# Kernel optimization log

Measured on AMD Instinct MI355X. Metric: run time of the kernel, lower is better.

## Reference

```python
import jax, jax.numpy as jnp
import numpy as np

B, H, L, N = 4, 256, 8192, 32  # batch, channels, seq_len, d_state//2 complex modes


def setup_inputs() -> dict:
    key = jax.random.key(0)
    ks = jax.random.split(key, 8)
    x = jax.random.normal(ks[0], (B, H, L), jnp.float32)
    # ChannelwiseLayerNorm params
    ln1_g = jnp.ones((H,), jnp.float32); ln1_b = jnp.zeros((H,), jnp.float32)
    ln2_g = jnp.ones((H,), jnp.float32); ln2_b = jnp.zeros((H,), jnp.float32)
    # S4D params (standard diagonal S4D init)
    log_dt = jax.random.uniform(ks[1], (H,), jnp.float32, np.log(1e-3), np.log(1e-1))
    log_A_real = jnp.log(0.5 * jnp.ones((H, N), jnp.float32))
    A_imag = jnp.tile(np.pi * jnp.arange(N, dtype=jnp.float32)[None, :], (H, 1))
    C_re = jax.random.normal(ks[2], (H, N), jnp.float32) * (0.5 ** 0.5)
    C_im = jax.random.normal(ks[3], (H, N), jnp.float32) * (0.5 ** 0.5)
    D = jax.random.normal(ks[4], (H,), jnp.float32)
    # 1x1 convs as dense matrices
    glu_w = jax.random.normal(ks[5], (2 * H, H), jnp.float32) * (1.0 / H) ** 0.5
    glu_b = jnp.zeros((2 * H,), jnp.float32)
    ffn_in_w = jax.random.normal(ks[6], (4 * H, H), jnp.float32) * (1.0 / H) ** 0.5
    ffn_in_b = jnp.zeros((4 * H,), jnp.float32)
    ffn_out_w = jax.random.normal(ks[7], (H, 4 * H), jnp.float32) * (1.0 / (4 * H)) ** 0.5
    ffn_out_b = jnp.zeros((H,), jnp.float32)
    return dict(x=x, ln1_g=ln1_g, ln1_b=ln1_b, ln2_g=ln2_g, ln2_b=ln2_b,
                log_dt=log_dt, log_A_real=log_A_real, A_imag=A_imag,
                C_re=C_re, C_im=C_im, D=D,
                glu_w=glu_w, glu_b=glu_b,
                ffn_in_w=ffn_in_w, ffn_in_b=ffn_in_b,
                ffn_out_w=ffn_out_w, ffn_out_b=ffn_out_b)


def _channel_ln(x, g, b, eps=1e-5):
    # normalize over channel dim (axis=1) of (B, C, L)
    mu = jnp.mean(x, axis=1, keepdims=True)
    var = jnp.var(x, axis=1, keepdims=True)
    return (x - mu) / jnp.sqrt(var + eps) * g[None, :, None] + b[None, :, None]


def _s4d(u, log_dt, log_A_real, A_imag, C_re, C_im, D):
    # u: (B, H, L); diagonal SSM via Vandermonde kernel + FFT conv
    Ls = u.shape[-1]
    dt = jnp.exp(log_dt)                       # (H,)
    A = -jnp.exp(log_A_real) + 1j * A_imag     # (H, N)
    dtA = A * dt[:, None]                      # (H, N)
    Cc = (C_re + 1j * C_im) * (jnp.exp(dtA) - 1.0) / A
    vand = jnp.exp(dtA[:, :, None] * jnp.arange(Ls))      # (H, N, L)
    K = 2.0 * jnp.einsum('hn,hnl->hl', Cc, vand).real     # (H, L)
    n = 2 * Ls
    y = jnp.fft.irfft(jnp.fft.rfft(u, n=n) * jnp.fft.rfft(K, n=n), n=n)[..., :Ls]
    return y + u * D[None, :, None]


def reference(x, ln1_g, ln1_b, ln2_g, ln2_b, log_dt, log_A_real, A_imag,
              C_re, C_im, D, glu_w, glu_b, ffn_in_w, ffn_in_b, ffn_out_w, ffn_out_b):
    # branch 1: norm -> S4D -> GELU -> 1x1 conv -> GLU -> residual
    y = _channel_ln(x, ln1_g, ln1_b)
    y = _s4d(y, log_dt, log_A_real, A_imag, C_re, C_im, D)
    y = jax.nn.gelu(y, approximate=False)
    y = jnp.einsum('oc,bcl->bol', glu_w, y) + glu_b[None, :, None]
    a, g = jnp.split(y, 2, axis=1)
    y = a * jax.nn.sigmoid(g)
    mid = x + y
    # branch 2: norm -> FFN (1x1 conv, GELU, 1x1 conv) -> residual
    y = _channel_ln(mid, ln2_g, ln2_b)
    y = jnp.einsum('oc,bcl->bol', ffn_in_w, y) + ffn_in_b[None, :, None]
    y = jax.nn.gelu(y, approximate=False)
    y = jnp.einsum('oc,bcl->bol', ffn_out_w, y) + ffn_out_b[None, :, None]
    return mid + y
```

## Files before the change

kernel.cpp:

```cpp
#include <hip/hip_runtime.h>
#include <hip/hip_bf16.h>

#define BB 4
#define HH 256
#define LL 8192
#define NN 32
#define CH 64
#define TT 128

typedef __attribute__((ext_vector_type(4))) float f32x4;
typedef __attribute__((ext_vector_type(8))) short s16x8;
typedef __attribute__((ext_vector_type(4))) short s16x4;
typedef unsigned int u32;

static __device__ __forceinline__ ushort f2bf(float f){
    union { float f; unsigned int i; } v; v.f = f;
    unsigned int x = v.i;
    return (ushort)((x + 0x7fffu + ((x >> 16) & 1u)) >> 16);
}

static __device__ __forceinline__ float fast_gelu(float x){
    float x3 = x*x*x;
    float z  = fmaf(0.03567740814f, x3, 0.7978845608f*x);
    float e  = __builtin_amdgcn_exp2f(z * 2.885390082f);
    float t  = 1.f - 2.f*__builtin_amdgcn_rcpf(e + 1.f);
    return 0.5f*x*(1.f + t);
}
static __device__ __forceinline__ float fast_sigmoid(float x){
    float e = __builtin_amdgcn_exp2f(-x * 1.442695041f);
    return __builtin_amdgcn_rcpf(1.f + e);
}

__global__ void k_prep_weights(const float* __restrict__ gw, const float* __restrict__ fiw,
                               const float* __restrict__ fow,
                               ushort* __restrict__ dglu, ushort* __restrict__ dfi,
                               ushort* __restrict__ dfo){
    int i = blockIdx.x * 256 + threadIdx.x;
    if (i < 512*256)  dglu[i] = f2bf(gw[i]);
    if (i < 1024*256) dfi[i]  = f2bf(fiw[i]);
    if (i < 1024*256) dfo[i]  = f2bf(fow[i]);
}

__global__ void k_scan_params(const float* __restrict__ log_dt, const float* __restrict__ log_A_real,
                              const float* __restrict__ A_imag, float4* __restrict__ out){
    int i = blockIdx.x * 256 + threadIdx.x;
    int h = i >> 5;
    float dt  = expf(log_dt[h]);
    float Are = -expf(log_A_real[i]);
    float Aim = A_imag[i];
    float xr = Are * dt, xi = Aim * dt;
    float er = expf(xr), sn, cs;
    sincosf(xi, &sn, &cs);
    float erT = expf(xr * (float)TT), snT, csT;
    sincosf(xi * (float)TT, &snT, &csT);
    out[i] = make_float4(er*cs, er*sn, erT*csT, erT*snT);
}

__global__ void __launch_bounds__(256) k_build(const float* __restrict__ log_dt,
      const float* __restrict__ log_A_real, const float* __restrict__ A_imag,
      const float* __restrict__ C_re, const float* __restrict__ C_im, const float* __restrict__ Dp,
      ushort* __restrict__ Tkb, ushort* __restrict__ M2b, ushort* __restrict__ V2b){
    int h = blockIdx.x, tid = threadIdx.x;
    __shared__ float prm[4][32];
    __shared__ float2 pw[129][32];
    __shared__ float kk[129];
    if (tid < 32){
        int n = tid, i = h*NN + n;
        float dt  = expf(log_dt[h]);
        float Are = -expf(log_A_real[i]);
        float Aim = A_imag[i];
        float xr = Are*dt, xi = Aim*dt;
        float er = expf(xr), sn, cs; sincosf(xi, &sn, &cs);
        float wre = er*cs, wim = er*sn;
        float nre = wre - 1.f, nim = wim;
        float inv = 1.f / (Are*Are + Aim*Aim);
        float qre = (nre*Are + nim*Aim) * inv;
        float qim = (nim*Are - nre*Aim) * inv;
        float cre = C_re[i], cim = C_im[i];
        prm[0][n] = xr; prm[1][n] = xi;
        prm[2][n] = 2.f*(cre*qre - cim*qim);
        prm[3][n] = 2.f*(cre*qim + cim*qre);
    }
    __syncthreads();
    if (tid < 129){
        float d = (float)tid, acc = 0.f;
        for (int n = 0; n < 32; ++n){
            float er = expf(prm[0][n]*d), sn, cs; sincosf(prm[1][n]*d, &sn, &cs);
            float pre = er*cs, pim = er*sn;
            pw[tid][n] = make_float2(pre, pim);
            acc += prm[2][n]*pre - prm[3][n]*pim;
        }
        kk[tid] = acc;
    }
    __syncthreads();
    float k0d = kk[0] + Dp[h];
    for (int idx = tid; idx < 128*128; idx += 256){
        int t = idx >> 7, ta = idx & 127, d = t - ta;
        float v = (d < 0) ? 0.f : ((d == 0) ? k0d : kk[d]);
        Tkb[(size_t)h*16384 + idx] = f2bf(v);
    }
    for (int idx = tid; idx < 128*64; idx += 256){
        int t = idx >> 6, j = idx & 63, n = j & 31;
        float2 p = pw[t+1][n];
        float v = (j < 32) ?  (prm[2][n]*p.x - prm[3][n]*p.y)
                           : -(prm[2][n]*p.y + prm[3][n]*p.x);
        M2b[(size_t)h*8192 + idx] = f2bf(v);
    }
    for (int idx = tid; idx < 64*128; idx += 256){
        int row = idx >> 7, ta = idx & 127, n = row & 31;
        float2 p = pw[127 - ta][n];
        V2b[(size_t)h*8192 + idx] = f2bf(row < 32 ? p.x : p.y);
    }
}

template<int MODE>
__global__ void __launch_bounds__(256) k_ln(const float* __restrict__ in, void* __restrict__ outp,
                     const float* __restrict__ gamma, const float* __restrict__ beta){
    int p = threadIdx.x & 63, cg = threadIdx.x >> 6;
    int b  = blockIdx.x / (LL/64);
    int l  = (blockIdx.x % (LL/64)) * 64 + p;
    const float* base = in + (size_t)b*HH*LL + l;
    int c0 = cg * 64;
    float s = 0.f, s2 = 0.f;
    #pragma unroll 8
    for (int j = 0; j < 64; ++j){
        float v = base[(size_t)(c0+j)*LL];
        s += v; s2 += v*v;
    }
    __shared__ float red[2][4][64];
    red[0][cg][p] = s; red[1][cg][p] = s2;
    __syncthreads();
    float ts = red[0][0][p]+red[0][1][p]+red[0][2][p]+red[0][3][p];
    float tq = red[1][0][p]+red[1][1][p]+red[1][2][p]+red[1][3][p];
    float mu   = ts * (1.f/HH);
    float var  = tq * (1.f/HH) - mu*mu;
    float rstd = rsqrtf(var + 1e-5f);
    if (MODE == 1){
        ushort* ob = (ushort*)outp + ((size_t)(b*LL + l))*HH + c0;
        #pragma unroll
        for (int j8 = 0; j8 < 8; ++j8){
            s16x8 v;
            #pragma unroll
            for (int e = 0; e < 8; ++e){
                int c = c0 + j8*8 + e;
                v[e] = (short)f2bf((base[(size_t)c*LL] - mu)*rstd*gamma[c] + beta[c]);
            }
            *(s16x8*)(ob + j8*8) = v;
        }
    } else {
        ushort* ob = (ushort*)outp + (size_t)b*HH*LL + l;
        #pragma unroll 8
        for (int j = 0; j < 64; ++j){
            int c = c0 + j;
            ob[(size_t)c*LL] = f2bf((base[(size_t)c*LL] - mu)*rstd*gamma[c] + beta[c]);
        }
    }
}

__global__ void __launch_bounds__(256) k_gemmA(const ushort* __restrict__ V2b,
                        const ushort* __restrict__ ub, float2* __restrict__ est){
    int bh = blockIdx.x, h = bh & (HH-1);
    int tid = threadIdx.x, wave = tid >> 6, lane = tid & 63;
    int m16 = lane & 15, kg = lane >> 4;
    const ushort* Vh = V2b + (size_t)h*8192;
    const ushort* ux = ub + (size_t)bh*LL;
    f32x4 acc[4] = {};
    #pragma unroll
    for (int k0 = 0; k0 < 128; k0 += 32){
        s16x8 fa = *(const s16x8*)&Vh[(wave*16 + m16)*128 + k0 + kg*8];
        #pragma unroll
        for (int nf = 0; nf < 4; ++nf){
            s16x8 fb = *(const s16x8*)&ux[(size_t)(nf*16 + m16)*128 + k0 + kg*8];
            acc[nf] = __builtin_amdgcn_mfma_f32_16x16x32_bf16(fa, fb, acc[nf], 0, 0, 0);
        }
    }
    #pragma unroll
    for (int nf = 0; nf < 4; ++nf){
        int c = nf*16 + m16;
        #pragma unroll
        for (int r = 0; r < 4; ++r){
            int srow = wave*16 + kg*4 + r;
            float* dst = (float*)&est[((size_t)bh*CH + c)*NN + (srow & 31)];
            dst[srow >> 5] = acc[nf][r];
        }
    }
}

__global__ void k_scan_B(const float4* __restrict__ par, const float2* __restrict__ est,
                         ushort* __restrict__ carr){
    int i = blockIdx.x * 256 + threadIdx.x;
    int n = i & 31, bh = i >> 5, h = bh & (HH-1);
    float4 p0 = par[h*NN + n];
    float wre = p0.z, wim = p0.w;
    float cre = 0.f, cim = 0.f;
    const float2* e = est + (size_t)bh*CH*NN + n;
    ushort* cb = carr + (size_t)bh*CH*64;
    for (int c = 0; c < CH; ++c){
        cb[c*64 + n]      = f2bf(cre);
        cb[c*64 + 32 + n] = f2bf(cim);
        float2 v = e[(size_t)c*NN];
        float nre = fmaf(wre, cre, fmaf(-wim, cim, v.x));
        float nim = fmaf(wre, cim, fmaf(wim, cre, v.y));
        cre = nre; cim = nim;
    }
}

__global__ void __launch_bounds__(256) k_gemmC(const ushort* __restrict__ Tkb,
                        const ushort* __restrict__ M2b, const ushort* __restrict__ ub,
                        const ushort* __restrict__ carr, ushort* __restrict__ gy){
    int bh = blockIdx.x, h = bh & (HH-1);
    int tid = threadIdx.x, wave = tid >> 6, lane = tid & 63;
    int m16 = lane & 15, kg = lane >> 4;
    const ushort* Th = Tkb + (size_t)h*16384;
    const ushort* Mh = M2b + (size_t)h*8192;
    const ushort* ux = ub + (size_t)bh*LL;
    const ushort* cb = carr + (size_t)bh*CH*64;
    f32x4 acc[2][4] = {};
    #pragma unroll
    for (int k0 = 0; k0 < 128; k0 += 32){
        s16x8 fa0 = *(const s16x8*)&Th[(size_t)(wave*32 + m16)*128 + k0 + kg*8];
        s16x8 fa1 = *(const s16x8*)&Th[(size_t)(wave*32 + 16 + m16)*128 + k0 + kg*8];
        #pragma unroll
        for (int nf = 0; nf < 4; ++nf){
            s16x8 fb = *(const s16x8*)&ux[(size_t)(nf*16 + m16)*128 + k0 + kg*8];
            acc[0][nf] = __builtin_amdgcn_mfma_f32_16x16x32_bf16(fa0, fb, acc[0][nf], 0, 0, 0);
            acc[1][nf] = __builtin_amdgcn_mfma_f32_16x16x32_bf16(fa1, fb, acc[1][nf], 0, 0, 0);
        }
    }
    #pragma unroll
    for (int k0 = 0; k0 < 64; k0 += 32){
        s16x8 fa0 = *(const s16x8*)&Mh[(wave*32 + m16)*64 + k0 + kg*8];
        s16x8 fa1 = *(const s16x8*)&Mh[(wave*32 + 16 + m16)*64 + k0 + kg*8];
        #pragma unroll
        for (int nf = 0; nf < 4; ++nf){
            s16x8 fb = *(const s16x8*)&cb[(nf*16 + m16)*64 + k0 + kg*8];
            acc[0][nf] = __builtin_amdgcn_mfma_f32_16x16x32_bf16(fa0, fb, acc[0][nf], 0, 0, 0);
            acc[1][nf] = __builtin_amdgcn_mfma_f32_16x16x32_bf16(fa1, fb, acc[1][nf], 0, 0, 0);
        }
    }
    #pragma unroll
    for (int mf = 0; mf < 2; ++mf){
        #pragma unroll
        for (int nf = 0; nf < 4; ++nf){
            int c = nf*16 + m16;
            int t0 = wave*32 + mf*16 + kg*4;
            s16x4 pk;
            #pragma unroll
            for (int r = 0; r < 4; ++r){
                pk[r] = (short)f2bf(fast_gelu(acc[mf][nf][r]));
            }
            *(s16x4*)&gy[(size_t)bh*LL + c*TT + t0] = pk;
        }
    }
}

__global__ void k_transpose(const ushort* __restrict__ in, ushort* __restrict__ out){
    __shared__ ushort tile[64][66];
    int tid = threadIdx.x;
    int lt = blockIdx.x, ht = blockIdx.y, b = blockIdx.z;
    const ushort* ib = in + ((size_t)b*HH + ht*64)*LL + lt*64;
    #pragma unroll
    for (int k = 0; k < 16; ++k){
        int j = tid + k*256;
        tile[j >> 6][j & 63] = ib[(size_t)(j >> 6)*LL + (j & 63)];
    }
    __syncthreads();
    ushort* obp = out + ((size_t)b*LL + lt*64)*HH + ht*64;
    #pragma unroll
    for (int k = 0; k < 16; ++k){
        int j = tid + k*256;
        obp[(size_t)(j >> 6)*HH + (j & 63)] = tile[j & 63][j >> 6];
    }
}

__global__ void __launch_bounds__(256) k_glu(const ushort* __restrict__ Wg, const ushort* __restrict__ Xt,
                     const float* __restrict__ x, const float* __restrict__ gb,
                     float* __restrict__ mid){
    __shared__ __align__(16) ushort sh[32768];
    int tid = threadIdx.x;
    int w = tid >> 6, lane = tid & 63;
    int m16 = lane & 15, kg = lane >> 4;
    int wr = w >> 1, wc = w & 1;
    int p0  = blockIdx.x * 128;
    int oa0 = blockIdx.y * 64;
    const ushort* Brow = Xt + (size_t)p0*256;
    int srow = lane >> 3;
    int scol = ((lane & 7) ^ (srow & 7)) * 8;
    f32x4 aa[2][4] = {}; f32x4 ag[2][4] = {};

    #define GSTAGE(buf, kt) { \
        int k0s = (kt)*64; \
        _Pragma("unroll") \
        for (int i = 0; i < 4; ++i){ \
            int rr = (w*4 + i)*8; \
            int grow = (rr < 64) ? (oa0 + rr + srow) : (256 + oa0 + (rr - 64) + srow); \
            __builtin_amdgcn_global_load_lds( \
                (const __attribute__((address_space(1))) u32*)(Wg + (size_t)grow*256 + k0s + scol), \
                (__attribute__((address_space(3))) u32*)&sh[(buf)*8192 + rr*64], 16, 0, 0); \
            __builtin_amdgcn_global_load_lds( \
                (const __attribute__((address_space(1))) u32*)(Brow + (size_t)(rr + srow)*256 + k0s + scol), \
                (__attribute__((address_space(3))) u32*)&sh[16384 + (buf)*8192 + rr*64], 16, 0, 0); \
        } }

    int buf = 0;
    GSTAGE(0, 0);
    __syncthreads();
    for (int kt = 0; kt < 4; ++kt){
        if (kt + 1 < 4) GSTAGE(buf^1, kt+1);
        #pragma unroll
        for (int k032 = 0; k032 < 64; k032 += 32){
            int c = (k032 >> 3) + kg;
            s16x8 fa[2], fg[2], fb[4];
            #pragma unroll
            for (int i = 0; i < 2; ++i){
                int ra = wr*32 + i*16 + m16;
                int rg = 64 + wr*32 + i*16 + m16;
                fa[i] = *(const s16x8*)&sh[buf*8192 + ra*64 + ((c ^ (ra & 7)) << 3)];
                fg[i] = *(const s16x8*)&sh[buf*8192 + rg*64 + ((c ^ (rg & 7)) << 3)];
            }
            #pragma unroll
            for (int i = 0; i < 4; ++i){
                int rb = wc*64 + i*16 + m16;
                fb[i] = *(const s16x8*)&sh[16384 + buf*8192 + rb*64 + ((c ^ (rb & 7)) << 3)];
            }
            #pragma unroll
            for (int mf = 0; mf < 2; ++mf){
                #pragma unroll
                for (int nf = 0; nf < 4; ++nf){
                    aa[mf][nf] = __builtin_amdgcn_mfma_f32_16x16x32_bf16(fa[mf], fb[nf], aa[mf][nf], 0, 0, 0);
                    ag[mf][nf] = __builtin_amdgcn_mfma_f32_16x16x32_bf16(fg[mf], fb[nf], ag[mf][nf], 0, 0, 0);
                }
            }
        }
        __syncthreads();
        buf ^= 1;
    }
    #undef GSTAGE

    #pragma unroll
    for (int mf = 0; mf < 2; ++mf){
        #pragma unroll
        for (int nf = 0; nf < 4; ++nf){
            int pc = p0 + wc*64 + nf*16 + m16;
            int b = pc >> 13, l = pc & (LL-1);
            #pragma unroll
            for (int r = 0; r < 4; ++r){
                int o = oa0 + wr*32 + mf*16 + kg*4 + r;
                float va  = aa[mf][nf][r] + gb[o];
                float vg  = ag[mf][nf][r] + gb[o + 256];
                float sig = fast_sigmoid(vg);
                size_t idx = ((size_t)(b*HH + o) << 13) + l;
                mid[idx] = x[idx] + va*sig;
            }
        }
    }
}

template<int KDIM, int EPI>
__global__ void __launch_bounds__(256) k_gemm_lds(const ushort* __restrict__ A,
                      const ushort* __restrict__ Bm, const float* __restrict__ bias,
                      const float* __restrict__ mid, void* __restrict__ Cout, int pbase){
    __shared__ __align__(16) ushort sh[32768];
    int tid = threadIdx.x;
    int w = tid >> 6, lane = tid & 63;
    int m16 = lane & 15, kg = lane >> 4;
    int wr = w >> 1, wc = w & 1;
    int q0  = blockIdx.x * 128;
    int oc0 = blockIdx.y * 128;
    const ushort* Arow = A  + (size_t)oc0*KDIM;
    const ushort* Brow = Bm + (size_t)q0*KDIM;
    int srow = lane >> 3;
    int scol = ((lane & 7) ^ (srow & 7)) * 8;
    f32x4 acc[4][4] = {};
    const int nK = KDIM/64;

    #define STAGE(buf, kt) { \
        int k0s = (kt)*64; \
        _Pragma("unroll") \
        for (int i = 0; i < 4; ++i){ \
            int rr = (w*4 + i)*8; \
            __builtin_amdgcn_global_load_lds( \
                (const __attribute__((address_space(1))) u32*)(Arow + (size_t)(rr + srow)*KDIM + k0s + scol), \
                (__attribute__((address_space(3))) u32*)&sh[(buf)*8192 + rr*64], 16, 0, 0); \
            __builtin_amdgcn_global_load_lds( \
                (const __attribute__((address_space(1))) u32*)(Brow + (size_t)(rr + srow)*KDIM + k0s + scol), \
                (__attribute__((address_space(3))) u32*)&sh[16384 + (buf)*8192 + rr*64], 16, 0, 0); \
        } }

    int buf = 0;
    STAGE(0, 0);
    __syncthreads();
    for (int kt = 0; kt < nK; ++kt){
        if (kt + 1 < nK) STAGE(buf^1, kt+1);
        #pragma unroll
        for (int k032 = 0; k032 < 64; k032 += 32){
            int c = (k032 >> 3) + kg;
            s16x8 af[4], bf[4];
            #pragma unroll
            for (int i = 0; i < 4; ++i){
                int ra = wr*64 + i*16 + m16;
                int rb = wc*64 + i*16 + m16;
                af[i] = *(const s16x8*)&sh[buf*8192 + ra*64 + ((c ^ (ra & 7)) << 3)];
                bf[i] = *(const s16x8*)&sh[16384 + buf*8192 + rb*64 + ((c ^ (rb & 7)) << 3)];
            }
            #pragma unroll
            for (int mf = 0; mf < 4; ++mf){
                #pragma unroll
                for (int nf = 0; nf < 4; ++nf)
                    acc[mf][nf] = __builtin_amdgcn_mfma_f32_16x16x32_bf16(af[mf], bf[nf], acc[mf][nf], 0, 0, 0);
            }
        }
        __syncthreads();
        buf ^= 1;
    }
    #undef STAGE

    if (EPI == 0){
        ushort (*lt)[136] = (ushort(*)[136])sh;
        #pragma unroll
        for (int mf = 0; mf < 4; ++mf){
            #pragma unroll
            for (int nf = 0; nf < 4; ++nf){
                int lr = wc*64 + nf*16 + m16;
                int lc = wr*64 + mf*16 + kg*4;
                s16x4 pk;
                #pragma unroll
                for (int r = 0; r < 4; ++r){
                    float v = acc[mf][nf][r] + bias[oc0 + lc + r];
                    pk[r] = (short)f2bf(fast_gelu(v));
                }
                *(s16x4*)&lt[lr][lc] = pk;
            }
        }
        __syncthreads();
        ushort* f1 = (ushort*)Cout;
        #pragma unroll
        for (int i = 0; i < 8; ++i){
            int chunk = i*256 + tid;
            int row = chunk >> 4, c16 = chunk & 15;
            s16x8 v = *(const s16x8*)&lt[row][c16*8];
            *(s16x8*)&f1[((size_t)(q0 + row) << 10) + oc0 + c16*8] = v;
        }
    } else {
        float* out = (float*)Cout;
        #pragma unroll
        for (int mf = 0; mf < 4; ++mf){
            #pragma unroll
            for (int nf = 0; nf < 4; ++nf){
                int pc = pbase + q0 + wc*64 + nf*16 + m16;
                int b = pc >> 13, l = pc & (LL-1);
                #pragma unroll
                for (int r = 0; r < 4; ++r){
                    int oc = oc0 + wr*64 + mf*16 + kg*4 + r;
                    size_t idx = ((size_t)(b*HH + oc) << 13) + l;
                    out[idx] = mid[idx] + acc[mf][nf][r] + bias[oc];
                }
            }
        }
    }
}

extern "C" void kernel_launch(void* const* d_in, const int* in_sizes, int n_in,
                              void* d_out, int out_size, void* d_ws, size_t ws_size,
                              hipStream_t stream) {
    const float* x          = (const float*)d_in[0];
    const float* ln1_g      = (const float*)d_in[1];
    const float* ln1_b      = (const float*)d_in[2];
    const float* ln2_g      = (const float*)d_in[3];
    const float* ln2_b      = (const float*)d_in[4];
    const float* log_dt     = (const float*)d_in[5];
    const float* log_A_real = (const float*)d_in[6];
    const float* A_imag     = (const float*)d_in[7];
    const float* C_re       = (const float*)d_in[8];
    const float* C_im       = (const float*)d_in[9];
    const float* Dv         = (const float*)d_in[10];
    const float* glu_w      = (const float*)d_in[11];
    const float* glu_b      = (const float*)d_in[12];
    const float* ffn_in_w   = (const float*)d_in[13];
    const float* ffn_in_b   = (const float*)d_in[14];
    const float* ffn_out_w  = (const float*)d_in[15];
    const float* ffn_out_b  = (const float*)d_in[16];
    float* out = (float*)d_out;

    char* ws = (char*)d_ws;
    const size_t MB = 1u << 20;
    float4* par  = (float4*)(ws);
    ushort* wglu = (ushort*)(ws + 256*1024);
    ushort* wfi  = (ushort*)(ws + 512*1024);
    ushort* wfo  = (ushort*)(ws + 1024*1024);
    ushort* Tkb  = (ushort*)(ws + 2*MB);
    ushort* M2b  = (ushort*)(ws + 10*MB);
    ushort* V2b  = (ushort*)(ws + 14*MB);
    ushort* ub   = (ushort*)(ws + 18*MB);
    float2* est  = (float2*)(ws + 34*MB);
    ushort* carr = (ushort*)(ws + 50*MB);
    ushort* gy   = (ushort*)(ws + 34*MB);
    ushort* gyt  = (ushort*)(ws + 50*MB);
    float*  mid  = (float*)(ws + 2*MB);
    ushort* x2t  = (ushort*)(ws + 36*MB);
    ushort* f1   = (ushort*)(ws + 52*MB);

    int G = (ws_size >= 117*MB) ? 4 : ((ws_size >= 85*MB) ? 2 : 1);

    k_prep_weights<<<1024, 256, 0, stream>>>(glu_w, ffn_in_w, ffn_out_w, wglu, wfi, wfo);
    k_scan_params<<<32, 256, 0, stream>>>(log_dt, log_A_real, A_imag, par);
    k_build<<<HH, 256, 0, stream>>>(log_dt, log_A_real, A_imag, C_re, C_im, Dv, Tkb, M2b, V2b);
    k_ln<2><<<BB*LL/64, 256, 0, stream>>>(x, ub, ln1_g, ln1_b);
    k_gemmA<<<BB*HH, 256, 0, stream>>>(V2b, ub, est);
    k_scan_B<<<BB*HH*NN/256, 256, 0, stream>>>(par, est, carr);
    k_gemmC<<<BB*HH, 256, 0, stream>>>(Tkb, M2b, ub, carr, gy);
    k_transpose<<<dim3(LL/64, HH/64, BB), 256, 0, stream>>>(gy, gyt);
    k_glu<<<dim3(BB*LL/128, 4), 256, 0, stream>>>(wglu, gyt, x, glu_b, mid);
    k_ln<1><<<BB*LL/64, 256, 0, stream>>>(mid, x2t, ln2_g, ln2_b);
    for (int b0 = 0; b0 < BB; b0 += G){
        int pbase = b0 * LL;
        k_gemm_lds<256,0><<<dim3(G*LL/128, 8), 256, 0, stream>>>(
            wfi, x2t + (size_t)pbase*256, ffn_in_b, nullptr, f1, 0);
        k_gemm_lds<1024,1><<<dim3(G*LL/128, 2), 256, 0, stream>>>(
            wfo, f1, ffn_out_b, mid, out, pbase);
    }
    (void)in_sizes; (void)n_in; (void)out_size; (void)ws_size;
}
```

Before: 304.6 us.

## Fuse FFN up and down projections into one kernel with LDS-resident hidden tile

Replaces the two tiled LDS GEMM launches (FFN-in with GELU, then FFN-out with residual) with one kernel. Each 512-thread block handles 64 positions: it computes the 1024-wide GELU hidden activations into a 128KB swizzled LDS buffer, then runs the down projection straight from LDS. This removes the global round trip of the bf16 hidden tensor and the batch-group launch loop. In exchange, operand A and B fragments are read directly from global memory without LDS staging or double buffering, and the large LDS footprint limits each CU to one block.

```diff
diff --git a/kernel.cpp b/kernel.cpp
--- a/kernel.cpp
+++ b/kernel.cpp
@@ -356,104 +356,83 @@
     }
 }
 
-template<int KDIM, int EPI>
-__global__ void __launch_bounds__(256) k_gemm_lds(const ushort* __restrict__ A,
-                      const ushort* __restrict__ Bm, const float* __restrict__ bias,
-                      const float* __restrict__ mid, void* __restrict__ Cout, int pbase){
-    __shared__ __align__(16) ushort sh[32768];
+__global__ void __launch_bounds__(512) k_ffn_fused(const ushort* __restrict__ W1,
+                      const ushort* __restrict__ W2, const ushort* __restrict__ Xt,
+                      const float* __restrict__ b1, const float* __restrict__ b2,
+                      const float* __restrict__ mid, float* __restrict__ out){
+    __shared__ __align__(16) ushort f1s[64*1024];
     int tid = threadIdx.x;
     int w = tid >> 6, lane = tid & 63;
     int m16 = lane & 15, kg = lane >> 4;
-    int wr = w >> 1, wc = w & 1;
-    int q0  = blockIdx.x * 128;
-    int oc0 = blockIdx.y * 128;
-    const ushort* Arow = A  + (size_t)oc0*KDIM;
-    const ushort* Brow = Bm + (size_t)q0*KDIM;
-    int srow = lane >> 3;
-    int scol = ((lane & 7) ^ (srow & 7)) * 8;
-    f32x4 acc[4][4] = {};
-    const int nK = KDIM/64;
-
-    #define STAGE(buf, kt) { \
-        int k0s = (kt)*64; \
-        _Pragma("unroll") \
-        for (int i = 0; i < 4; ++i){ \
-            int rr = (w*4 + i)*8; \
-            __builtin_amdgcn_global_load_lds( \
-                (const __attribute__((address_space(1))) u32*)(Arow + (size_t)(rr + srow)*KDIM + k0s + scol), \
-                (__attribute__((address_space(3))) u32*)&sh[(buf)*8192 + rr*64], 16, 0, 0); \
-            __builtin_amdgcn_global_load_lds( \
-                (const __attribute__((address_space(1))) u32*)(Brow + (size_t)(rr + srow)*KDIM + k0s + scol), \
-                (__attribute__((address_space(3))) u32*)&sh[16384 + (buf)*8192 + rr*64], 16, 0, 0); \
-        } }
-
-    int buf = 0;
-    STAGE(0, 0);
-    __syncthreads();
-    for (int kt = 0; kt < nK; ++kt){
-        if (kt + 1 < nK) STAGE(buf^1, kt+1);
-        #pragma unroll
-        for (int k032 = 0; k032 < 64; k032 += 32){
-            int c = (k032 >> 3) + kg;
-            s16x8 af[4], bf[4];
-            #pragma unroll
-            for (int i = 0; i < 4; ++i){
-                int ra = wr*64 + i*16 + m16;
-                int rb = wc*64 + i*16 + m16;
-                af[i] = *(const s16x8*)&sh[buf*8192 + ra*64 + ((c ^ (ra & 7)) << 3)];
-                bf[i] = *(const s16x8*)&sh[16384 + buf*8192 + rb*64 + ((c ^ (rb & 7)) << 3)];
-            }
-            #pragma unroll
-            for (int mf = 0; mf < 4; ++mf){
+    int p0 = blockIdx.x * 64;
+
+    {
+        int o1 = w*128;
+        f32x4 acc[8][4] = {};
+        #pragma unroll
+        for (int k0 = 0; k0 < 256; k0 += 32){
+            s16x8 fb[4];
+            #pragma unroll
+            for (int nf = 0; nf < 4; ++nf)
+                fb[nf] = *(const s16x8*)&Xt[(size_t)(p0 + nf*16 + m16)*256 + k0 + kg*8];
+            #pragma unroll
+            for (int mf = 0; mf < 8; ++mf){
+                s16x8 fa = *(const s16x8*)&W1[(size_t)(o1 + mf*16 + m16)*256 + k0 + kg*8];
                 #pragma unroll
                 for (int nf = 0; nf < 4; ++nf)
-                    acc[mf][nf] = __builtin_amdgcn_mfma_f32_16x16x32_bf16(af[mf], bf[nf], acc[mf][nf], 0, 0, 0);
-            }
-        }
-        __syncthreads();
-        buf ^= 1;
-    }
-    #undef STAGE
-
-    if (EPI == 0){
-        ushort (*lt)[136] = (ushort(*)[136])sh;
-        #pragma unroll
-        for (int mf = 0; mf < 4; ++mf){
+                    acc[mf][nf] = __builtin_amdgcn_mfma_f32_16x16x32_bf16(fa, fb[nf], acc[mf][nf], 0, 0, 0);
+            }
+        }
+        #pragma unroll
+        for (int mf = 0; mf < 8; ++mf){
             #pragma unroll
             for (int nf = 0; nf < 4; ++nf){
-                int lr = wc*64 + nf*16 + m16;
-                int lc = wr*64 + mf*16 + kg*4;
+                int pos = nf*16 + m16;
+                int oc  = o1 + mf*16 + kg*4;
                 s16x4 pk;
                 #pragma unroll
-                for (int r = 0; r < 4; ++r){
-                    float v = acc[mf][nf][r] + bias[oc0 + lc + r];
-                    pk[r] = (short)f2bf(fast_gelu(v));
-                }
-                *(s16x4*)&lt[lr][lc] = pk;
-            }
-        }
-        __syncthreads();
-        ushort* f1 = (ushort*)Cout;
-        #pragma unroll
-        for (int i = 0; i < 8; ++i){
-            int chunk = i*256 + tid;
-            int row = chunk >> 4, c16 = chunk & 15;
-            s16x8 v = *(const s16x8*)&lt[row][c16*8];
-            *(s16x8*)&f1[((size_t)(q0 + row) << 10) + oc0 + c16*8] = v;
-        }
-    } else {
-        float* out = (float*)Cout;
-        #pragma unroll
-        for (int mf = 0; mf < 4; ++mf){
+                for (int r = 0; r < 4; ++r)
+                    pk[r] = (short)f2bf(fast_gelu(acc[mf][nf][r] + b1[oc + r]));
+                int c8  = oc >> 3;
+                int swz = (c8 & ~7) | ((c8 ^ pos) & 7);
+                *(s16x4*)&f1s[pos*1024 + swz*8 + (oc & 7)] = pk;
+            }
+        }
+    }
+    __syncthreads();
+
+    {
+        int o2 = w*32;
+        f32x4 acc[2][4] = {};
+        #pragma unroll 4
+        for (int k0 = 0; k0 < 1024; k0 += 32){
+            s16x8 fb[4];
             #pragma unroll
             for (int nf = 0; nf < 4; ++nf){
-                int pc = pbase + q0 + wc*64 + nf*16 + m16;
+                int pos = nf*16 + m16;
+                int c8  = (k0 >> 3) + kg;
+                int swz = (c8 & ~7) | ((c8 ^ pos) & 7);
+                fb[nf] = *(const s16x8*)&f1s[pos*1024 + swz*8];
+            }
+            #pragma unroll
+            for (int mf = 0; mf < 2; ++mf){
+                s16x8 fa = *(const s16x8*)&W2[(size_t)(o2 + mf*16 + m16)*1024 + k0 + kg*8];
+                #pragma unroll
+                for (int nf = 0; nf < 4; ++nf)
+                    acc[mf][nf] = __builtin_amdgcn_mfma_f32_16x16x32_bf16(fa, fb[nf], acc[mf][nf], 0, 0, 0);
+            }
+        }
+        #pragma unroll
+        for (int mf = 0; mf < 2; ++mf){
+            #pragma unroll
+            for (int nf = 0; nf < 4; ++nf){
+                int pc = p0 + nf*16 + m16;
                 int b = pc >> 13, l = pc & (LL-1);
                 #pragma unroll
                 for (int r = 0; r < 4; ++r){
-                    int oc = oc0 + wr*64 + mf*16 + kg*4 + r;
+                    int oc = o2 + mf*16 + kg*4 + r;
                     size_t idx = ((size_t)(b*HH + oc) << 13) + l;
-                    out[idx] = mid[idx] + acc[mf][nf][r] + bias[oc];
+                    out[idx] = mid[idx] + acc[mf][nf][r] + b2[oc];
                 }
             }
         }
@@ -498,9 +477,6 @@
     ushort* gyt  = (ushort*)(ws + 50*MB);
     float*  mid  = (float*)(ws + 2*MB);
     ushort* x2t  = (ushort*)(ws + 36*MB);
-    ushort* f1   = (ushort*)(ws + 52*MB);
-
-    int G = (ws_size >= 117*MB) ? 4 : ((ws_size >= 85*MB) ? 2 : 1);
 
     k_prep_weights<<<1024, 256, 0, stream>>>(glu_w, ffn_in_w, ffn_out_w, wglu, wfi, wfo);
     k_scan_params<<<32, 256, 0, stream>>>(log_dt, log_A_real, A_imag, par);
@@ -512,12 +488,6 @@
     k_transpose<<<dim3(LL/64, HH/64, BB), 256, 0, stream>>>(gy, gyt);
     k_glu<<<dim3(BB*LL/128, 4), 256, 0, stream>>>(wglu, gyt, x, glu_b, mid);
     k_ln<1><<<BB*LL/64, 256, 0, stream>>>(mid, x2t, ln2_g, ln2_b);
-    for (int b0 = 0; b0 < BB; b0 += G){
-        int pbase = b0 * LL;
-        k_gemm_lds<256,0><<<dim3(G*LL/128, 8), 256, 0, stream>>>(
-            wfi, x2t + (size_t)pbase*256, ffn_in_b, nullptr, f1, 0);
-        k_gemm_lds<1024,1><<<dim3(G*LL/128, 2), 256, 0, stream>>>(
-            wfo, f1, ffn_out_b, mid, out, pbase);
-    }
+    k_ffn_fused<<<BB*LL/64, 512, 0, stream>>>(wfi, wfo, x2t, ffn_in_b, ffn_out_b, mid, out);
     (void)in_sizes; (void)n_in; (void)out_size; (void)ws_size;
 }
```

Measured after the change: 348.4 us. 14.4% more time.
